# Kernel optimization log

Measured on AMD Instinct MI355X. Metric: run time of the kernel, lower is better.

## Reference

```python
import jax, jax.numpy as jnp
import numpy as np

N_NODES, N_EDGES, IN_F = 20000, 320000, 64
H1, H2 = 2, 2          # attn heads per GATv2 layer
D1, D2 = 128, 128      # gnn_size per layer
NM = [128, 128]        # nodemlp hidden sizes
EM = [512, 256]        # edgemlp hidden sizes
OUT_F = 1
NEG_SLOPE = 0.2


def _lin_init(key, fan_in, fan_out):
    kw, kb = jax.random.split(key)
    s = 1.0 / np.sqrt(fan_in)
    return (jax.random.uniform(kw, (fan_in, fan_out), jnp.float32, -s, s),
            jax.random.uniform(kb, (fan_out,), jnp.float32, -s, s))


def setup_inputs() -> dict:
    key = jax.random.key(0)
    ks = jax.random.split(key, 16)
    x = jax.random.normal(ks[0], (N_NODES, IN_F), jnp.float32)
    src = jax.random.randint(ks[1], (N_EDGES,), 0, N_NODES, jnp.int32)
    dst = jax.random.randint(ks[2], (N_EDGES,), 0, N_NODES, jnp.int32)
    # NodeMLP
    nw0, nb0 = _lin_init(ks[3], IN_F, NM[0])
    nw1, nb1 = _lin_init(ks[4], NM[0], NM[1])
    # GATv2 layer 1 (in=IN_F -> H1*D1)
    g1ws, g1bs = _lin_init(ks[5], IN_F, H1 * D1)
    g1wd, g1bd = _lin_init(ks[6], IN_F, H1 * D1)
    g1a = jax.random.normal(ks[7], (H1, D1), jnp.float32) * (1.0 / np.sqrt(D1))
    # GATv2 layer 2 (in=H1*D1 -> H2*D2)
    g2ws, g2bs = _lin_init(ks[8], H1 * D1, H2 * D2)
    g2wd, g2bd = _lin_init(ks[9], H1 * D1, H2 * D2)
    g2a = jax.random.normal(ks[10], (H2, D2), jnp.float32) * (1.0 / np.sqrt(D2))
    # EdgeMLP: in = 2*(NM[-1] + H2*D2) = 768
    e_in = 2 * (NM[-1] + H2 * D2)
    ew0, eb0 = _lin_init(ks[11], e_in, EM[0])
    ew1, eb1 = _lin_init(ks[12], EM[0], EM[1])
    ew2, eb2 = _lin_init(ks[13], EM[1], OUT_F)
    return dict(x=x, src=src, dst=dst,
                nw0=nw0, nb0=nb0, nw1=nw1, nb1=nb1,
                g1ws=g1ws, g1bs=g1bs, g1wd=g1wd, g1bd=g1bd, g1a=g1a,
                g2ws=g2ws, g2bs=g2bs, g2wd=g2wd, g2bd=g2bd, g2a=g2a,
                ew0=ew0, eb0=eb0, ew1=ew1, eb1=eb1, ew2=ew2, eb2=eb2)


def _segment_softmax(logits, dst, n):
    # logits: (E, H); softmax over edges sharing the same dst node
    m = jax.ops.segment_max(logits, dst, num_segments=n)
    e = jnp.exp(logits - m[dst])
    s = jax.ops.segment_sum(e, dst, num_segments=n)
    return e / s[dst]


def _gatv2(h, src, dst, ws, bs, wd, bd, attn, heads, dim, n):
    fs = (h @ ws + bs).reshape(n, heads, dim)   # fc_src
    fd = (h @ wd + bd).reshape(n, heads, dim)   # fc_dst
    e = jax.nn.leaky_relu(fs[src] + fd[dst], NEG_SLOPE)      # (E,H,D)
    logits = jnp.einsum('ehd,hd->eh', e, attn)               # (E,H)
    a = _segment_softmax(logits, dst, n)                      # (E,H)
    out = jax.ops.segment_sum(a[..., None] * fs[src], dst, num_segments=n)
    return jax.nn.relu(out).reshape(n, heads * dim)           # flatten heads


def reference(x, src, dst,
              nw0, nb0, nw1, nb1,
              g1ws, g1bs, g1wd, g1bd, g1a,
              g2ws, g2bs, g2wd, g2bd, g2a,
              ew0, eb0, ew1, eb1, ew2, eb2):
    n = x.shape[0]
    # NodeMLP (dropout=0 -> identity)
    h1 = jax.nn.relu(x @ nw0 + nb0)
    h1 = jax.nn.relu(h1 @ nw1 + nb1)
    # GCN: two GATv2Conv layers with relu activation, heads flattened
    h2 = _gatv2(x, src, dst, g1ws, g1bs, g1wd, g1bd, g1a, H1, D1, n)
    h2 = _gatv2(h2, src, dst, g2ws, g2bs, g2wd, g2bd, g2a, H2, D2, n)
    # EdgeMLP: gather src/dst, concat, MLP (relu before every layer but first)
    h = jnp.concatenate([h1[src], h1[dst], h2[src], h2[dst]], axis=1)  # (E,768)
    h = h @ ew0 + eb0
    h = jax.nn.relu(h) @ ew1 + eb1
    h = jax.nn.relu(h) @ ew2 + eb2
    return h  # (E, 1) edge scores
```

## Files before the change

### kernel.cpp

```cpp
#include <hip/hip_runtime.h>
#include <hip/hip_bf16.h>

constexpr int N_NODES = 20000;
constexpr int N_EDGES = 320000;

typedef _Float16 half8 __attribute__((ext_vector_type(8)));
typedef float    f32x16 __attribute__((ext_vector_type(16)));

__device__ __forceinline__ float lrelu(float x) { return x > 0.f ? x : 0.2f * x; }

__global__ void hist_kernel(const int* __restrict__ dst, int* __restrict__ counts) {
    int e = blockIdx.x * 256 + threadIdx.x;
    if (e < N_EDGES) atomicAdd(&counts[dst[e]], 1);
}

__global__ void scan_all_kernel(const int* __restrict__ counts,
                                int* __restrict__ row_off, int* __restrict__ cursor) {
    __shared__ int ps[1024];
    const int t = threadIdx.x;
    const int base = t * 20;
    int loc[20];
    int sum = 0;
#pragma unroll
    for (int i = 0; i < 20; ++i) {
        const int idx = base + i;
        const int v = (idx < N_NODES) ? counts[idx] : 0;
        loc[i] = sum;
        sum += v;
    }
    ps[t] = sum;
    __syncthreads();
    for (int off = 1; off < 1024; off <<= 1) {
        const int v = (t >= off) ? ps[t - off] : 0;
        __syncthreads();
        ps[t] += v;
        __syncthreads();
    }
    const int ex = ps[t] - sum;
#pragma unroll
    for (int i = 0; i < 20; ++i) {
        const int idx = base + i;
        if (idx < N_NODES) {
            row_off[idx] = ex + loc[i];
            cursor[idx]  = ex + loc[i];
        }
    }
    if (t == 0) row_off[N_NODES] = N_EDGES;
}

__global__ void scatter_kernel(const int* __restrict__ src, const int* __restrict__ dst,
                               int* __restrict__ cursor, int* __restrict__ eidx,
                               int* __restrict__ srcs) {
    int e = blockIdx.x * 256 + threadIdx.x;
    if (e < N_EDGES) {
        int p = atomicAdd(&cursor[dst[e]], 1);
        eidx[p] = e;
        srcs[p] = src[e];
    }
}

template <int K, int M>
__device__ __forceinline__ void pack_one(int idx, const float* __restrict__ W,
                                         int r1, int k1, int r2, int joff, int ldw,
                                         _Float16* __restrict__ H,
                                         _Float16* __restrict__ L) {
    const int l  = idx & 63;
    const int t  = (idx >> 6) % (M / 32);
    const int s  = (idx >> 6) / (M / 32);
    const int j  = joff + t * 32 + (l & 31);
    const int kb = s * 16 + (l >> 5) * 8;
    half8 vh, vl;
#pragma unroll
    for (int i = 0; i < 8; ++i) {
        const int k    = kb + i;
        const int rrow = (k < k1) ? (r1 + k) : (r2 + (k - k1));
        const float w  = W[(size_t)rrow * ldw + j];
        const _Float16 h = (_Float16)w;
        vh[i] = h;
        vl[i] = (_Float16)(w - (float)h);
    }
    reinterpret_cast<half8*>(H)[idx] = vh;
    reinterpret_cast<half8*>(L)[idx] = vl;
}

constexpr int OFF_W1  = 0;
constexpr int OFF_G1S = 16384;
constexpr int OFF_G1D = 18432;
constexpr int OFF_G2S = 20480;
constexpr int OFF_G2D = 28672;
constexpr int OFF_SW0 = 36864;
constexpr int OFF_SW1 = 49152;
constexpr int OFF_DW0 = 61440;
constexpr int OFF_DW1 = 73728;
constexpr int OFF_N0  = 86016;
constexpr int OFF_N1  = 87040;
constexpr int PACK_TOT = 89088;

struct PackIn {
    const float *ew1, *g1ws, *g1wd, *g2ws, *g2wd, *ew0, *nw0, *nw1;
    _Float16 *H, *L;
};

__global__ void prepack_all_kernel(PackIn a) {
    const int idx = blockIdx.x * 256 + threadIdx.x;
    if (idx >= PACK_TOT) return;
    _Float16* H = a.H;
    _Float16* L = a.L;
    if (idx < OFF_G1S)
        pack_one<512, 256>(idx - OFF_W1, a.ew1, 0, 512, 0, 0, 256,
                           H + OFF_W1 * 8, L + OFF_W1 * 8);
    else if (idx < OFF_G1D)
        pack_one<64, 256>(idx - OFF_G1S, a.g1ws, 0, 64, 0, 0, 256,
                          H + OFF_G1S * 8, L + OFF_G1S * 8);
    else if (idx < OFF_G2S)
        pack_one<64, 256>(idx - OFF_G1D, a.g1wd, 0, 64, 0, 0, 256,
                          H + OFF_G1D * 8, L + OFF_G1D * 8);
    else if (idx < OFF_G2D)
        pack_one<256, 256>(idx - OFF_G2S, a.g2ws, 0, 256, 0, 0, 256,
                           H + OFF_G2S * 8, L + OFF_G2S * 8);
    else if (idx < OFF_SW0)
        pack_one<256, 256>(idx - OFF_G2D, a.g2wd, 0, 256, 0, 0, 256,
                           H + OFF_G2D * 8, L + OFF_G2D * 8);
    else if (idx < OFF_SW1)
        pack_one<384, 256>(idx - OFF_SW0, a.ew0, 0, 128, 256, 0, 512,
                           H + OFF_SW0 * 8, L + OFF_SW0 * 8);
    else if (idx < OFF_DW0)
        pack_one<384, 256>(idx - OFF_SW1, a.ew0, 0, 128, 256, 256, 512,
                           H + OFF_SW1 * 8, L + OFF_SW1 * 8);
    else if (idx < OFF_DW1)
        pack_one<384, 256>(idx - OFF_DW0, a.ew0, 128, 128, 512, 0, 512,
                           H + OFF_DW0 * 8, L + OFF_DW0 * 8);
    else if (idx < OFF_N0)
        pack_one<384, 256>(idx - OFF_DW1, a.ew0, 128, 128, 512, 256, 512,
                           H + OFF_DW1 * 8, L + OFF_DW1 * 8);
    else if (idx < OFF_N1)
        pack_one<64, 128>(idx - OFF_N0, a.nw0, 0, 64, 0, 0, 128,
                          H + OFF_N0 * 8, L + OFF_N0 * 8);
    else
        pack_one<128, 128>(idx - OFF_N1, a.nw1, 0, 128, 0, 0, 128,
                           H + OFF_N1 * 8, L + OFF_N1 * 8);
}

struct LinOut { float* y[4]; const float* b[4]; };

template <int K, int TJ, int WR, int K1, int LD1, int LD2, int LDY,
          bool RELU, int MINW, int SEG>
__global__ __launch_bounds__(256, MINW) void mfma_linear2_kernel(
    const float* __restrict__ X1, const float* __restrict__ X2,
    const _Float16* __restrict__ BHp, const _Float16* __restrict__ BLp,
    LinOut lo, int N) {
    constexpr int WC    = 4 / WR;
    constexpr int TILES = WC * TJ;
    const int jb  = blockIdx.y;
    const int tid = threadIdx.x;
    const int wv  = tid >> 6, l = tid & 63;
    const int rg  = (WR == 1) ? 0 : (wv & 1);
    const int cg  = (WR == 1) ? wv : (wv >> 1);
    const int m   = l & 31, h = l >> 5;
    const int row = blockIdx.x * (32 * WR) + rg * 32 + m;
    const int ar  = (row < N) ? row : (N - 1);
    const float* __restrict__ xr1 = X1 + (size_t)ar * LD1;
    const float* __restrict__ xr2 = X2 + (size_t)ar * LD2;
    const half8* __restrict__ BH = reinterpret_cast<const half8*>(BHp) + (size_t)jb * SEG;
    const half8* __restrict__ BL = reinterpret_cast<const half8*>(BLp) + (size_t)jb * SEG;
    const float* __restrict__ bp = lo.b[jb];
    float* __restrict__ Y = lo.y[jb];

    f32x16 acc[TJ];
#pragma unroll
    for (int jt = 0; jt < TJ; ++jt) {
        const float bv = bp ? bp[cg * TJ * 32 + jt * 32 + m] : 0.f;
#pragma unroll
        for (int r = 0; r < 16; ++r) acc[jt][r] = bv;
    }

    const int kf = h * 8;
    const float* pf = (kf < K1) ? (xr1 + kf) : (xr2 + (kf - K1));
    float4 xa = *reinterpret_cast<const float4*>(pf);
    float4 xb = *reinterpret_cast<const float4*>(pf + 4);

    for (int s = 0; s < K / 16; ++s) {
        const float xs[8] = {xa.x, xa.y, xa.z, xa.w, xb.x, xb.y, xb.z, xb.w};
        if (s + 1 < K / 16) {
            const int kn = (s + 1) * 16 + h * 8;
            const float* pn = (kn < K1) ? (xr1 + kn) : (xr2 + (kn - K1));
            xa = *reinterpret_cast<const float4*>(pn);
            xb = *reinterpret_cast<const float4*>(pn + 4);
        }
        half8 ah, al;
#pragma unroll
        for (int i = 0; i < 8; ++i) {
            const _Float16 hi = (_Float16)xs[i];
            ah[i] = hi;
            al[i] = (_Float16)(xs[i] - (float)hi);
        }
#pragma unroll
        for (int jt = 0; jt < TJ; ++jt) {
            const int fi = (s * TILES + cg * TJ + jt) * 64 + l;
            const half8 bh = BH[fi];
            const half8 bl = BL[fi];
            acc[jt] = __builtin_amdgcn_mfma_f32_32x32x16_f16(ah, bh, acc[jt], 0, 0, 0);
            acc[jt] = __builtin_amdgcn_mfma_f32_32x32x16_f16(al, bh, acc[jt], 0, 0, 0);
            acc[jt] = __builtin_amdgcn_mfma_f32_32x32x16_f16(ah, bl, acc[jt], 0, 0, 0);
        }
    }

    const int rbase = blockIdx.x * (32 * WR) + rg * 32;
#pragma unroll
    for (int jt = 0; jt < TJ; ++jt) {
        const int j = cg * TJ * 32 + jt * 32 + m;
#pragma unroll
        for (int r = 0; r < 16; ++r) {
            const int orow = rbase + (r & 3) + 8 * (r >> 2) + 4 * h;
            if (orow < N) {
                float v = acc[jt][r];
                if (RELU) v = fmaxf(v, 0.f);
                Y[(size_t)orow * LDY + j] = v;
            }
        }
    }
}

__global__ void gat_fused_kernel(const float* __restrict__ fs, const float* __restrict__ fd,
                                 const float* __restrict__ attn,
                                 const int* __restrict__ row_off,
                                 const int* __restrict__ srcs,
                                 float* __restrict__ outp) {
    const int wv = threadIdx.x >> 6, l = threadIdx.x & 63;
    const int n = blockIdx.x * 4 + wv;
    if (n >= N_NODES) return;
    const int base = (l >> 5) * 128 + (l & 31) * 4;
    const float4 fdv = *reinterpret_cast<const float4*>(&fd[n * 256 + base]);
    const float4 av  = *reinterpret_cast<const float4*>(&attn[base]);
    const int s0 = row_off[n], s1 = row_off[n + 1];

    float m = -INFINITY, lsum = 0.f;
    float4 acc = {0.f, 0.f, 0.f, 0.f};
    float4 v0 = {0,0,0,0}, v1 = {0,0,0,0};
    if (s0 < s1)
        v0 = *reinterpret_cast<const float4*>(&fs[(size_t)srcs[s0] * 256 + base]);
    if (s0 + 1 < s1)
        v1 = *reinterpret_cast<const float4*>(&fs[(size_t)srcs[s0 + 1] * 256 + base]);
    for (int i = s0; i < s1; ++i) {
        const float4 vc = v0;
        v0 = v1;
        if (i + 2 < s1)
            v1 = *reinterpret_cast<const float4*>(&fs[(size_t)srcs[i + 2] * 256 + base]);
        float p = lrelu(vc.x + fdv.x) * av.x;
        p = fmaf(lrelu(vc.y + fdv.y), av.y, p);
        p = fmaf(lrelu(vc.z + fdv.z), av.z, p);
        p = fmaf(lrelu(vc.w + fdv.w), av.w, p);
#pragma unroll
        for (int off = 1; off < 32; off <<= 1) p += __shfl_xor(p, off);
        const float mn = fmaxf(m, p);
        const float alpha = __expf(m - mn);
        const float w = __expf(p - mn);
        lsum = fmaf(lsum, alpha, w);
        acc.x = fmaf(acc.x, alpha, w * vc.x);
        acc.y = fmaf(acc.y, alpha, w * vc.y);
        acc.z = fmaf(acc.z, alpha, w * vc.z);
        acc.w = fmaf(acc.w, alpha, w * vc.w);
        m = mn;
    }
    const float inv = (s1 > s0) ? 1.f / lsum : 0.f;
    float4 o;
    o.x = fmaxf(acc.x * inv, 0.f);
    o.y = fmaxf(acc.y * inv, 0.f);
    o.z = fmaxf(acc.z * inv, 0.f);
    o.w = fmaxf(acc.w * inv, 0.f);
    *reinterpret_cast<float4*>(&outp[n * 256 + base]) = o;
}

__global__ __launch_bounds__(256, 2) void edge_mlp6_kernel(
    const float* __restrict__ S, const float* __restrict__ Dn,
    const int* __restrict__ srcs, const int* __restrict__ eidx,
    const int* __restrict__ dstf,
    const _Float16* __restrict__ WpH,
    const float* __restrict__ b1, const float* __restrict__ w2,
    const float* __restrict__ b2, float* __restrict__ out) {
    __shared__ __align__(16) _Float16 Bs[2][8][512];
    const int tid = threadIdx.x;
    const int wv  = tid >> 6, l = tid & 63;
    const int m   = l & 31, h = l >> 5;
    const int e0  = blockIdx.x * 128;
    const int slot = e0 + wv * 32 + m;
    const float* __restrict__ Srow = S  + (size_t)srcs[slot] * 512;
    const float* __restrict__ Drow = Dn + (size_t)dstf[eidx[slot]] * 512;

    f32x16 acc[8];
#pragma unroll
    for (int jt = 0; jt < 8; ++jt) {
        const float bv = b1[jt * 32 + m];
#pragma unroll
        for (int r = 0; r < 16; ++r) acc[jt][r] = bv;
    }

#pragma unroll
    for (int c = 0; c < 2; ++c) {
        const int jt = wv * 2 + c;
        *reinterpret_cast<float4*>(&Bs[0][jt][l * 8]) =
            *reinterpret_cast<const float4*>(WpH + ((size_t)jt * 64 + l) * 8);
    }
    float4 sa = *reinterpret_cast<const float4*>(Srow + h * 8);
    float4 sb = *reinterpret_cast<const float4*>(Srow + h * 8 + 4);
    float4 da = *reinterpret_cast<const float4*>(Drow + h * 8);
    float4 db = *reinterpret_cast<const float4*>(Drow + h * 8 + 4);
    __syncthreads();

    for (int s = 0; s < 32; ++s) {
        const int buf = s & 1;
        float4 bst[2];
        if (s < 31) {
#pragma unroll
            for (int c = 0; c < 2; ++c) {
                const int jt = wv * 2 + c;
                bst[c] = *reinterpret_cast<const float4*>(
                    WpH + ((size_t)((s + 1) * 8 + jt) * 64 + l) * 8);
            }
        }
        const float xs[8] = {sa.x + da.x, sa.y + da.y, sa.z + da.z, sa.w + da.w,
                             sb.x + db.x, sb.y + db.y, sb.z + db.z, sb.w + db.w};
        if (s < 31) {
            const int ko = (s + 1) * 16 + h * 8;
            sa = *reinterpret_cast<const float4*>(Srow + ko);
            sb = *reinterpret_cast<const float4*>(Srow + ko + 4);
            da = *reinterpret_cast<const float4*>(Drow + ko);
            db = *reinterpret_cast<const float4*>(Drow + ko + 4);
        }
        half8 ah, al;
#pragma unroll
        for (int i = 0; i < 8; ++i) {
            const float xv = fmaxf(xs[i], 0.f);
            const _Float16 hi = (_Float16)xv;
            ah[i] = hi;
            al[i] = (_Float16)(xv - (float)hi);
        }
#pragma unroll
        for (int jt = 0; jt < 8; ++jt) {
            const half8 bh = *reinterpret_cast<const half8*>(&Bs[buf][jt][l * 8]);
            acc[jt] = __builtin_amdgcn_mfma_f32_32x32x16_f16(ah, bh, acc[jt], 0, 0, 0);
            acc[jt] = __builtin_amdgcn_mfma_f32_32x32x16_f16(al, bh, acc[jt], 0, 0, 0);
        }
        if (s < 31) {
#pragma unroll
            for (int c = 0; c < 2; ++c) {
                const int jt = wv * 2 + c;
                *reinterpret_cast<float4*>(&Bs[buf ^ 1][jt][l * 8]) = bst[c];
            }
        }
        __syncthreads();
    }

    float part[16];
#pragma unroll
    for (int r = 0; r < 16; ++r) part[r] = 0.f;
#pragma unroll
    for (int jt = 0; jt < 8; ++jt) {
        const float w2v = w2[jt * 32 + m];
#pragma unroll
        for (int r = 0; r < 16; ++r)
            part[r] = fmaf(fmaxf(acc[jt][r], 0.f), w2v, part[r]);
    }
#pragma unroll
    for (int off = 1; off < 32; off <<= 1)
#pragma unroll
        for (int r = 0; r < 16; ++r) part[r] += __shfl_xor(part[r], off);
    if (m == 0) {
        const float b2v = b2[0];
#pragma unroll
        for (int r = 0; r < 16; ++r) {
            const int row = (r & 3) + 8 * (r >> 2) + 4 * h;
            out[eidx[e0 + wv * 32 + row]] = part[r] + b2v;
        }
    }
}

extern "C" void kernel_launch(void* const* d_in, const int* in_sizes, int n_in,
                              void* d_out, int out_size, void* d_ws, size_t ws_size,
                              hipStream_t stream) {
    (void)in_sizes; (void)n_in; (void)out_size; (void)ws_size;
    const float* x    = (const float*)d_in[0];
    const int*   src  = (const int*)d_in[1];
    const int*   dst  = (const int*)d_in[2];
    const float* nw0  = (const float*)d_in[3];
    const float* nb0  = (const float*)d_in[4];
    const float* nw1  = (const float*)d_in[5];
    const float* nb1  = (const float*)d_in[6];
    const float* g1ws = (const float*)d_in[7];
    const float* g1bs = (const float*)d_in[8];
    const float* g1wd = (const float*)d_in[9];
    const float* g1bd = (const float*)d_in[10];
    const float* g1a  = (const float*)d_in[11];
    const float* g2ws = (const float*)d_in[12];
    const float* g2bs = (const float*)d_in[13];
    const float* g2wd = (const float*)d_in[14];
    const float* g2bd = (const float*)d_in[15];
    const float* g2a  = (const float*)d_in[16];
    const float* ew0  = (const float*)d_in[17];
    const float* eb0  = (const float*)d_in[18];
    const float* ew1  = (const float*)d_in[19];
    const float* eb1  = (const float*)d_in[20];
    const float* ew2  = (const float*)d_in[21];
    const float* eb2  = (const float*)d_in[22];
    float* out = (float*)d_out;

    float* wsF = (float*)d_ws;
    float* h1  = wsF;
    float* g2o = wsF + 2560000;
    float* fsb = wsF + 7680000;
    float* fdb = wsF + 12800000;
    float* g1o = wsF + 17920000;
    float* Sb  = wsF + 7680000;
    float* Db  = wsF + 17920000;
    int* wsI     = (int*)(wsF + 28160000);
    int* row_off = wsI;
    int* cursor  = wsI + 20016;
    int* eidx    = wsI + 40032;
    int* srcs    = wsI + 360032;
    _Float16* pkH = (_Float16*)((char*)d_ws + 115361280);
    _Float16* pkL = pkH + (size_t)PACK_TOT * 8;

    hipMemsetAsync(cursor, 0, N_NODES * sizeof(int), stream);
    hist_kernel<<<1250, 256, 0, stream>>>(dst, cursor);
    scan_all_kernel<<<1, 1024, 0, stream>>>(cursor, row_off, cursor);
    scatter_kernel<<<1250, 256, 0, stream>>>(src, dst, cursor, eidx, srcs);

    PackIn pin{ew1, g1ws, g1wd, g2ws, g2wd, ew0, nw0, nw1, pkH, pkL};
    prepack_all_kernel<<<(PACK_TOT + 255) / 256, 256, 0, stream>>>(pin);

    {   LinOut lo{{fsb, nullptr, nullptr, nullptr}, {nb0, nullptr, nullptr, nullptr}};
        mfma_linear2_kernel<64, 1, 1, 64, 64, 64, 128, true, 4, 0>
            <<<dim3(625, 1), 256, 0, stream>>>(x, x, pkH + OFF_N0 * 8, pkL + OFF_N0 * 8,
                                               lo, N_NODES); }
    {   LinOut lo{{h1, nullptr, nullptr, nullptr}, {nb1, nullptr, nullptr, nullptr}};
        mfma_linear2_kernel<128, 1, 1, 128, 128, 128, 128, true, 4, 0>
            <<<dim3(625, 1), 256, 0, stream>>>(fsb, fsb, pkH + OFF_N1 * 8, pkL + OFF_N1 * 8,
                                               lo, N_NODES); }

    {   LinOut lo{{fsb, fdb, nullptr, nullptr}, {g1bs, g1bd, nullptr, nullptr}};
        mfma_linear2_kernel<64, 2, 1, 64, 64, 64, 256, false, 4, 2048>
            <<<dim3(625, 2), 256, 0, stream>>>(x, x, pkH + OFF_G1S * 8, pkL + OFF_G1S * 8,
                                               lo, N_NODES); }
    gat_fused_kernel<<<5000, 256, 0, stream>>>(fsb, fdb, g1a, row_off, srcs, g1o);

    {   LinOut lo{{fsb, fdb, nullptr, nullptr}, {g2bs, g2bd, nullptr, nullptr}};
        mfma_linear2_kernel<256, 2, 1, 256, 256, 256, 256, false, 4, 8192>
            <<<dim3(625, 2), 256, 0, stream>>>(g1o, g1o, pkH + OFF_G2S * 8, pkL + OFF_G2S * 8,
                                               lo, N_NODES); }
    gat_fused_kernel<<<5000, 256, 0, stream>>>(fsb, fdb, g2a, row_off, srcs, g2o);

    {   LinOut lo{{Sb, Sb + 256, Db, Db + 256}, {nullptr, nullptr, eb0, eb0 + 256}};
        mfma_linear2_kernel<384, 4, 2, 128, 128, 256, 512, false, 2, 12288>
            <<<dim3(313, 4), 256, 0, stream>>>(h1, g2o, pkH + OFF_SW0 * 8, pkL + OFF_SW0 * 8,
                                               lo, N_NODES); }

    edge_mlp6_kernel<<<N_EDGES / 128, 256, 0, stream>>>(Sb, Db, srcs, eidx, dst,
                                                        pkH + OFF_W1 * 8,
                                                        eb1, ew2, eb2, out);
}
```

Baseline: 623.7 us.

## Store GAT source features in fp16 and retile large node linears

The source-feature projection of both GAT layers is now written as fp16 into a separate buffer, and the gather-heavy attention kernel reads half4 instead of float4. This halves gathered bytes per edge in the memory-bound aggregation. Separately, the layer-2 GAT linear and the edge-MLP first-layer linear switch to a WR=4 layout (four row groups, each wave covering all 8 column tiles) with fewer blocks. That changes register pressure and occupancy. The fp16 storage adds rounding error to the source features used in logits and aggregation.

```diff
diff --git a/kernel.cpp b/kernel.cpp
--- a/kernel.cpp
+++ b/kernel.cpp
@@ -5,6 +5,7 @@
 constexpr int N_EDGES = 320000;
 
 typedef _Float16 half8 __attribute__((ext_vector_type(8)));
+typedef _Float16 half4 __attribute__((ext_vector_type(4)));
 typedef float    f32x16 __attribute__((ext_vector_type(16)));
 
 __device__ __forceinline__ float lrelu(float x) { return x > 0.f ? x : 0.2f * x; }
@@ -141,7 +142,7 @@
                            H + OFF_N1 * 8, L + OFF_N1 * 8);
 }
 
-struct LinOut { float* y[4]; const float* b[4]; };
+struct LinOut { float* y[4]; const float* b[4]; _Float16* yh[4]; };
 
 template <int K, int TJ, int WR, int K1, int LD1, int LD2, int LDY,
           bool RELU, int MINW, int SEG>
@@ -154,8 +155,8 @@
     const int jb  = blockIdx.y;
     const int tid = threadIdx.x;
     const int wv  = tid >> 6, l = tid & 63;
-    const int rg  = (WR == 1) ? 0 : (wv & 1);
-    const int cg  = (WR == 1) ? wv : (wv >> 1);
+    const int rg  = (WR == 1) ? 0 : ((WR == 4) ? wv : (wv & 1));
+    const int cg  = (WR == 1) ? wv : ((WR == 4) ? 0 : (wv >> 1));
     const int m   = l & 31, h = l >> 5;
     const int row = blockIdx.x * (32 * WR) + rg * 32 + m;
     const int ar  = (row < N) ? row : (N - 1);
@@ -165,6 +166,7 @@
     const half8* __restrict__ BL = reinterpret_cast<const half8*>(BLp) + (size_t)jb * SEG;
     const float* __restrict__ bp = lo.b[jb];
     float* __restrict__ Y = lo.y[jb];
+    _Float16* __restrict__ Yh = lo.yh[jb];
 
     f32x16 acc[TJ];
 #pragma unroll
@@ -215,13 +217,15 @@
             if (orow < N) {
                 float v = acc[jt][r];
                 if (RELU) v = fmaxf(v, 0.f);
-                Y[(size_t)orow * LDY + j] = v;
+                if (Y)  Y[(size_t)orow * LDY + j] = v;
+                if (Yh) Yh[(size_t)orow * LDY + j] = (_Float16)v;
             }
         }
     }
 }
 
-__global__ void gat_fused_kernel(const float* __restrict__ fs, const float* __restrict__ fd,
+__global__ void gat_fused_kernel(const _Float16* __restrict__ fsh,
+                                 const float* __restrict__ fd,
                                  const float* __restrict__ attn,
                                  const int* __restrict__ row_off,
                                  const int* __restrict__ srcs,
@@ -236,16 +240,16 @@
 
     float m = -INFINITY, lsum = 0.f;
     float4 acc = {0.f, 0.f, 0.f, 0.f};
-    float4 v0 = {0,0,0,0}, v1 = {0,0,0,0};
+    half4 v0 = {0, 0, 0, 0}, v1 = {0, 0, 0, 0};
     if (s0 < s1)
-        v0 = *reinterpret_cast<const float4*>(&fs[(size_t)srcs[s0] * 256 + base]);
+        v0 = *reinterpret_cast<const half4*>(&fsh[(size_t)srcs[s0] * 256 + base]);
     if (s0 + 1 < s1)
-        v1 = *reinterpret_cast<const float4*>(&fs[(size_t)srcs[s0 + 1] * 256 + base]);
+        v1 = *reinterpret_cast<const half4*>(&fsh[(size_t)srcs[s0 + 1] * 256 + base]);
     for (int i = s0; i < s1; ++i) {
-        const float4 vc = v0;
+        const float4 vc = {(float)v0.x, (float)v0.y, (float)v0.z, (float)v0.w};
         v0 = v1;
         if (i + 2 < s1)
-            v1 = *reinterpret_cast<const float4*>(&fs[(size_t)srcs[i + 2] * 256 + base]);
+            v1 = *reinterpret_cast<const half4*>(&fsh[(size_t)srcs[i + 2] * 256 + base]);
         float p = lrelu(vc.x + fdv.x) * av.x;
         p = fmaf(lrelu(vc.y + fdv.y), av.y, p);
         p = fmaf(lrelu(vc.z + fdv.z), av.z, p);
@@ -412,6 +416,7 @@
     float* g1o = wsF + 17920000;
     float* Sb  = wsF + 7680000;
     float* Db  = wsF + 17920000;
+    _Float16* fsh = (_Float16*)(wsF + 23040000);
     int* wsI     = (int*)(wsF + 28160000);
     int* row_off = wsI;
     int* cursor  = wsI + 20016;
@@ -428,30 +433,35 @@
     PackIn pin{ew1, g1ws, g1wd, g2ws, g2wd, ew0, nw0, nw1, pkH, pkL};
     prepack_all_kernel<<<(PACK_TOT + 255) / 256, 256, 0, stream>>>(pin);
 
-    {   LinOut lo{{fsb, nullptr, nullptr, nullptr}, {nb0, nullptr, nullptr, nullptr}};
+    {   LinOut lo{{fsb, nullptr, nullptr, nullptr}, {nb0, nullptr, nullptr, nullptr},
+                  {nullptr, nullptr, nullptr, nullptr}};
         mfma_linear2_kernel<64, 1, 1, 64, 64, 64, 128, true, 4, 0>
             <<<dim3(625, 1), 256, 0, stream>>>(x, x, pkH + OFF_N0 * 8, pkL + OFF_N0 * 8,
                                                lo, N_NODES); }
-    {   LinOut lo{{h1, nullptr, nullptr, nullptr}, {nb1, nullptr, nullptr, nullptr}};
+    {   LinOut lo{{h1, nullptr, nullptr, nullptr}, {nb1, nullptr, nullptr, nullptr},
+                  {nullptr, nullptr, nullptr, nullptr}};
         mfma_linear2_kernel<128, 1, 1, 128, 128, 128, 128, true, 4, 0>
             <<<dim3(625, 1), 256, 0, stream>>>(fsb, fsb, pkH + OFF_N1 * 8, pkL + OFF_N1 * 8,
                                                lo, N_NODES); }
 
-    {   LinOut lo{{fsb, fdb, nullptr, nullptr}, {g1bs, g1bd, nullptr, nullptr}};
+    {   LinOut lo{{nullptr, fdb, nullptr, nullptr}, {g1bs, g1bd, nullptr, nullptr},
+                  {fsh, nullptr, nullptr, nullptr}};
         mfma_linear2_kernel<64, 2, 1, 64, 64, 64, 256, false, 4, 2048>
             <<<dim3(625, 2), 256, 0, stream>>>(x, x, pkH + OFF_G1S * 8, pkL + OFF_G1S * 8,
                                                lo, N_NODES); }
-    gat_fused_kernel<<<5000, 256, 0, stream>>>(fsb, fdb, g1a, row_off, srcs, g1o);
-
-    {   LinOut lo{{fsb, fdb, nullptr, nullptr}, {g2bs, g2bd, nullptr, nullptr}};
-        mfma_linear2_kernel<256, 2, 1, 256, 256, 256, 256, false, 4, 8192>
-            <<<dim3(625, 2), 256, 0, stream>>>(g1o, g1o, pkH + OFF_G2S * 8, pkL + OFF_G2S * 8,
+    gat_fused_kernel<<<5000, 256, 0, stream>>>(fsh, fdb, g1a, row_off, srcs, g1o);
+
+    {   LinOut lo{{nullptr, fdb, nullptr, nullptr}, {g2bs, g2bd, nullptr, nullptr},
+                  {fsh, nullptr, nullptr, nullptr}};
+        mfma_linear2_kernel<256, 8, 4, 256, 256, 256, 256, false, 2, 8192>
+            <<<dim3(157, 2), 256, 0, stream>>>(g1o, g1o, pkH + OFF_G2S * 8, pkL + OFF_G2S * 8,
                                                lo, N_NODES); }
-    gat_fused_kernel<<<5000, 256, 0, stream>>>(fsb, fdb, g2a, row_off, srcs, g2o);
-
-    {   LinOut lo{{Sb, Sb + 256, Db, Db + 256}, {nullptr, nullptr, eb0, eb0 + 256}};
-        mfma_linear2_kernel<384, 4, 2, 128, 128, 256, 512, false, 2, 12288>
-            <<<dim3(313, 4), 256, 0, stream>>>(h1, g2o, pkH + OFF_SW0 * 8, pkL + OFF_SW0 * 8,
+    gat_fused_kernel<<<5000, 256, 0, stream>>>(fsh, fdb, g2a, row_off, srcs, g2o);
+
+    {   LinOut lo{{Sb, Sb + 256, Db, Db + 256}, {nullptr, nullptr, eb0, eb0 + 256},
+                  {nullptr, nullptr, nullptr, nullptr}};
+        mfma_linear2_kernel<384, 8, 4, 128, 128, 256, 512, false, 2, 12288>
+            <<<dim3(157, 4), 256, 0, stream>>>(h1, g2o, pkH + OFF_SW0 * 8, pkL + OFF_SW0 * 8,
                                                lo, N_NODES); }
 
     edge_mlp6_kernel<<<N_EDGES / 128, 256, 0, stream>>>(Sb, Db, srcs, eidx, dst,
```

After: 628.7 us. No clear change (+0.8%).
